# Performance work log

Measured on AMD Instinct MI355X. Metric: run time of the kernel, lower is better.

The kernel has to match this reference:

```python
import jax, jax.numpy as jnp
import numpy as np

B, H, A, T, C, MAXLEN = 128, 512, 128, 256, 256, 300
NEG_SLOPE = 0.01  # torch LeakyReLU default


def setup_inputs() -> dict:
    key = jax.random.key(0)
    ks = jax.random.split(key, 32)
    s = 0.02
    inp = {
        "key": jax.random.normal(ks[0], (B, A, T), jnp.float32),
        "value": jax.random.normal(ks[1], (B, T, A), jnp.float32),
        "Yinput": jax.random.randint(ks[2], (B, MAXLEN), 0, C),
        "frame_lens": jax.random.randint(ks[3], (B,), 1024, 2049),
        "max_len": MAXLEN,
        # parameters
        "emb": jax.random.normal(ks[4], (C, H), jnp.float32) * s,   # tied with projection
        "Wq": jax.random.normal(ks[5], (A, H), jnp.float32) * s,
        "bq": jnp.zeros((A,), jnp.float32),
        "Wih1": jax.random.normal(ks[6], (4 * H, H + A), jnp.float32) * s,
        "Whh1": jax.random.normal(ks[7], (4 * H, H), jnp.float32) * s,
        "bih1": jnp.zeros((4 * H,), jnp.float32),
        "bhh1": jnp.zeros((4 * H,), jnp.float32),
        "Wih2": jax.random.normal(ks[8], (4 * H, H), jnp.float32) * s,
        "Whh2": jax.random.normal(ks[9], (4 * H, H), jnp.float32) * s,
        "bih2": jnp.zeros((4 * H,), jnp.float32),
        "bhh2": jnp.zeros((4 * H,), jnp.float32),
        "Wih3": jax.random.normal(ks[10], (4 * H, H), jnp.float32) * s,
        "Whh3": jax.random.normal(ks[11], (4 * H, H), jnp.float32) * s,
        "bih3": jnp.zeros((4 * H,), jnp.float32),
        "bhh3": jnp.zeros((4 * H,), jnp.float32),
        "Wmlp": jax.random.normal(ks[12], (H, H + A), jnp.float32) * s,
        "bmlp": jnp.zeros((H,), jnp.float32),
        "bproj": jnp.zeros((C,), jnp.float32),
        "h00": jax.random.normal(ks[13], (1, H), jnp.float32) * s,
        "h01": jax.random.normal(ks[14], (1, H), jnp.float32) * s,
        "h02": jax.random.normal(ks[15], (1, H), jnp.float32) * s,
        "c00": jax.random.normal(ks[16], (1, H), jnp.float32) * s,
        "c01": jax.random.normal(ks[17], (1, H), jnp.float32) * s,
        "c02": jax.random.normal(ks[18], (1, H), jnp.float32) * s,
    }
    return inp


def _lstm_cell(x, h, c, Wih, Whh, bih, bhh):
    gates = x @ Wih.T + bih + h @ Whh.T + bhh  # [B,4H]
    i, f, g, o = jnp.split(gates, 4, axis=-1)
    i, f, o = jax.nn.sigmoid(i), jax.nn.sigmoid(f), jax.nn.sigmoid(o)
    g = jnp.tanh(g)
    c_new = f * c + i * g
    h_new = o * jnp.tanh(c_new)
    return h_new, c_new


def _attend(key, value, h, Wq, bq, mask):
    q = h @ Wq.T + bq                       # [B,A]
    energy = jnp.einsum('ba,bat->bt', q, key)  # [B,T]
    attn = jax.nn.softmax(energy, axis=-1)
    attn = attn * mask
    attn = attn / jnp.sum(attn, axis=-1, keepdims=True)
    ctx = jnp.einsum('bt,btv->bv', attn, value)  # [B,A]
    return ctx


def reference(key, value, Yinput, frame_lens, max_len,
              emb, Wq, bq,
              Wih1, Whh1, bih1, bhh1,
              Wih2, Whh2, bih2, bhh2,
              Wih3, Whh3, bih3, bhh3,
              Wmlp, bmlp, bproj,
              h00, h01, h02, c00, c01, c02):
    b, _, t = key.shape
    flens = frame_lens // 8
    mask = (jnp.arange(t)[None, :] < flens[:, None]).astype(key.dtype)  # [B,T]

    bc = lambda p: jnp.broadcast_to(p, (b, p.shape[-1]))
    h1, h2, h3 = bc(h00), bc(h01), bc(h02)
    c1, c2, c3 = bc(c00), bc(c01), bc(c02)
    ctx = _attend(key, value, h3, Wq, bq, mask)

    def step(carry, y_t):
        h1, h2, h3, c1, c2, c3, ctx = carry
        x = jnp.concatenate([emb[y_t], ctx], axis=-1)       # [B, H+A]
        h1, c1 = _lstm_cell(x, h1, c1, Wih1, Whh1, bih1, bhh1)
        h2, c2 = _lstm_cell(h1, h2, c2, Wih2, Whh2, bih2, bhh2)
        h3, c3 = _lstm_cell(h2, h3, c3, Wih3, Whh3, bih3, bhh3)
        ctx = _attend(key, value, h3, Wq, bq, mask)
        cat = jnp.concatenate([h3, ctx], axis=-1)           # [B, H+A]
        m = cat @ Wmlp.T + bmlp
        m = jnp.where(m >= 0, m, NEG_SLOPE * m)             # LeakyReLU
        logits = m @ emb.T + bproj                          # tied projection
        pred = jax.nn.log_softmax(logits, axis=-1)          # [B,C]
        return (h1, h2, h3, c1, c2, c3, ctx), pred

    ys = Yinput[:, :max_len].T                              # [max_len, B]
    _, preds = jax.lax.scan(step, (h1, h2, h3, c1, c2, c3, ctx), ys)
    return jnp.transpose(preds, (1, 0, 2))                  # [B, max_len, C]
```

## Files before the change

kernel.cpp:

```cpp
#include <hip/hip_runtime.h>

typedef unsigned short u16;
typedef unsigned int   u32;
typedef __bf16 bf16x8 __attribute__((ext_vector_type(8)));
typedef float  f32x4  __attribute__((ext_vector_type(4)));

#define NB 128
#define NH 512
#define NA 128
#define NT 256
#define NC 256
#define NL 300

static constexpr size_t OFF_BAR   = 0;
static constexpr size_t OFF_H1    = 4096;
static constexpr size_t OFF_H2    = OFF_H1   + 262144;
static constexpr size_t OFF_H3    = OFF_H2   + 262144;
static constexpr size_t OFF_C     = OFF_H3   + 262144;
static constexpr size_t OFF_CTX   = OFF_C    + 786432;
static constexpr size_t OFF_Q     = OFF_CTX  + 32768;
static constexpr size_t OFF_MP    = OFF_Q    + 65536;
static constexpr size_t OFF_M     = OFF_MP   + 262144;
static constexpr size_t OFF_LOG   = OFF_M    + 131072;
static constexpr size_t OFF_W1C   = OFF_LOG  + 131072;
static constexpr size_t OFF_WHH1  = OFF_W1C  + 524288;
static constexpr size_t OFF_WIH2  = OFF_WHH1 + 2097152;
static constexpr size_t OFF_WHH2  = OFF_WIH2 + 2097152;
static constexpr size_t OFF_WIH3  = OFF_WHH2 + 2097152;
static constexpr size_t OFF_WHH3  = OFF_WIH3 + 2097152;
static constexpr size_t OFF_WMH   = OFF_WHH3 + 2097152;
static constexpr size_t OFF_WMC   = OFF_WMH  + 524288;
static constexpr size_t OFF_WQ    = OFF_WMC  + 131072;
static constexpr size_t OFF_EMB   = OFF_WQ   + 131072;
static constexpr size_t OFF_PROJ1 = OFF_EMB  + 262144;
static constexpr size_t OFF_BS2   = OFF_PROJ1+ 1048576;
static constexpr size_t OFF_BS3   = OFF_BS2  + 8192;
static constexpr size_t OFF_KEY   = OFF_BS3  + 8192;
static constexpr size_t OFF_VAL   = OFF_KEY  + 8388608;
static constexpr size_t OFF_END   = OFF_VAL  + 8388608;

__device__ __forceinline__ u16 f2bf(float f) {
  u32 u = __builtin_bit_cast(u32, f);
  u32 r = (u + 0x7FFFu + ((u >> 16) & 1u)) >> 16;
  return (u16)r;
}
__device__ __forceinline__ float bf2f(u16 h) {
  return __builtin_bit_cast(float, ((u32)h) << 16);
}
__device__ __forceinline__ float sigm(float x) { return 1.f / (1.f + __expf(-x)); }
__device__ __forceinline__ float ftanh(float x) {
  x = fminf(fmaxf(x, -15.f), 15.f);
  float e = __expf(2.f * x);
  return (e - 1.f) / (e + 1.f);
}

__device__ __forceinline__ float ld_coh_f32(const float* p) {
  float v;
  asm volatile("global_load_dword %0, %1, off sc0 sc1\n\ts_waitcnt vmcnt(0)"
               : "=v"(v) : "v"(p) : "memory");
  return v;
}
__device__ __forceinline__ u32 ld_coh_u32(const u32* p) {
  u32 v;
  asm volatile("global_load_dword %0, %1, off sc0 sc1\n\ts_waitcnt vmcnt(0)"
               : "=v"(v) : "v"(p) : "memory");
  return v;
}
__device__ __forceinline__ f32x4 ld_coh16(const u16* p) {
  f32x4 v;
  asm volatile("global_load_dwordx4 %0, %1, off sc0 sc1\n\ts_waitcnt vmcnt(0)"
               : "=v"(v) : "v"(p) : "memory");
  return v;
}
__device__ __forceinline__ void ld_coh64(const u16* p, f32x4& a, f32x4& b, f32x4& c, f32x4& d) {
  asm volatile(
      "global_load_dwordx4 %0, %4, off sc0 sc1\n\t"
      "global_load_dwordx4 %1, %4, off offset:16 sc0 sc1\n\t"
      "global_load_dwordx4 %2, %4, off offset:32 sc0 sc1\n\t"
      "global_load_dwordx4 %3, %4, off offset:48 sc0 sc1\n\t"
      "s_waitcnt vmcnt(0)"
      : "=&v"(a), "=&v"(b), "=&v"(c), "=&v"(d)
      : "v"(p) : "memory");
}
__device__ __forceinline__ void st_coh_f32(float* p, float v) {
  asm volatile("global_store_dword %0, %1, off sc0 sc1" :: "v"(p), "v"(v) : "memory");
}
__device__ __forceinline__ void st_coh_bf16(u16* p, u16 v) {
  u32 vv = v;
  asm volatile("global_store_short %0, %1, off sc0 sc1" :: "v"(p), "v"(vv) : "memory");
}

__device__ __forceinline__ void gbar(char* ws, int xcd, u32& phase) {
  asm volatile("s_waitcnt vmcnt(0)" ::: "memory");
  __syncthreads();
  if (threadIdx.x == 0) {
    u32* cx = (u32*)(ws + OFF_BAR + 256 * (size_t)(1 + xcd));
    u32* cr = (u32*)(ws + OFF_BAR);
    ++phase;
    u32 prev = __hip_atomic_fetch_add(cx, 1u, __ATOMIC_RELAXED, __HIP_MEMORY_SCOPE_AGENT);
    if (prev == phase * 32u - 1u)
      __hip_atomic_fetch_add(cr, 1u, __ATOMIC_RELAXED, __HIP_MEMORY_SCOPE_AGENT);
    u32 tgt = phase * 8u;
    while (ld_coh_u32(cr) < tgt) __builtin_amdgcn_s_sleep(2);
  }
  __syncthreads();
}

__device__ __forceinline__ float wgmax(float v, float* s) {
#pragma unroll
  for (int o = 32; o; o >>= 1) v = fmaxf(v, __shfl_xor(v, o, 64));
  if ((threadIdx.x & 63) == 0) s[threadIdx.x >> 6] = v;
  __syncthreads();
  v = fmaxf(fmaxf(s[0], s[1]), fmaxf(s[2], s[3]));
  __syncthreads();
  return v;
}
__device__ __forceinline__ float wgsum(float v, float* s) {
#pragma unroll
  for (int o = 32; o; o >>= 1) v += __shfl_xor(v, o, 64);
  if ((threadIdx.x & 63) == 0) s[threadIdx.x >> 6] = v;
  __syncthreads();
  v = s[0] + s[1] + s[2] + s[3];
  __syncthreads();
  return v;
}

__device__ __forceinline__ void stage512(u16* sA, int lstride, int lcol0, const u16* src, int mt) {
  const int row = threadIdx.x >> 4;
  const int c4  = (threadIdx.x & 15) * 32;
  const u16* p = src + (((size_t)(mt * 16 + row)) << 9) + c4;
  f32x4 a, b, c, d;
  ld_coh64(p, a, b, c, d);
  f32x4* dst = (f32x4*)(sA + (size_t)row * lstride + lcol0 + c4);
  dst[0] = a; dst[1] = b; dst[2] = c; dst[3] = d;
}
__device__ __forceinline__ void stage128(u16* sA, int lstride, int lcol0, const u16* src, int mt) {
  const int row = threadIdx.x >> 4;
  const int c1  = (threadIdx.x & 15) * 8;
  const u16* p = src + (size_t)(mt * 16 + row) * 128 + c1;
  f32x4 a = ld_coh16(p);
  *(f32x4*)(sA + (size_t)row * lstride + lcol0 + c1) = a;
}

template <int NKS>
__device__ __forceinline__ f32x4 mm_part(f32x4 acc, const u16* sAp, int lstride, int lcol0,
                                         int ks0, const u16* W, int kw, int colbase, int lane) {
  const int ra = lane & 15, kg = lane >> 4;
  const u16* ap = sAp + (size_t)ra * lstride + lcol0 + kg * 8 + ks0 * 32;
  const u16* wp = W + (size_t)(colbase + ra) * kw + kg * 8 + (size_t)ks0 * 32;
#pragma unroll
  for (int k = 0; k < NKS; ++k) {
    bf16x8 av = *(const bf16x8*)(ap + k * 32);
    bf16x8 bv = *(const bf16x8*)(wp + k * 32);
    acc = __builtin_amdgcn_mfma_f32_16x16x32_bf16(av, bv, acc, 0, 0, 0);
  }
  return acc;
}
__device__ __forceinline__ void gx_write(float (*gx)[16][17], int wv, int lane, f32x4 acc) {
  const int col = lane & 15, r0 = (lane >> 4) * 4;
#pragma unroll
  for (int r = 0; r < 4; ++r) gx[wv][r0 + r][col] = acc[r];
}
__device__ __forceinline__ float gx_sum(float (*gx)[16][17], int bl, int jl) {
  return gx[0][bl][jl] + gx[1][bl][jl] + gx[2][bl][jl] + gx[3][bl][jl];
}

__device__ __forceinline__ void cell_update(int layer, int mt, int ut, int t,
                                            float (*gx)[16][17], const int* Yin,
                                            const u16* proj1, const float* bsum,
                                            float* CB, u16* hout) {
  const int bl = threadIdx.x >> 4, ul = threadIdx.x & 15;
  const int bg = mt * 16 + bl, ug = ut * 16 + ul;
  float iv = gx[0][bl][ul], fv = gx[1][bl][ul], gv = gx[2][bl][ul], ov = gx[3][bl][ul];
  if (proj1) {
    const int y = Yin[bg * NL + t];
    const u16* pr = proj1 + (size_t)y * 2048 + ug;
    iv += bf2f(pr[0]); fv += bf2f(pr[512]); gv += bf2f(pr[1024]); ov += bf2f(pr[1536]);
  } else {
    iv += bsum[ug]; fv += bsum[512 + ug]; gv += bsum[1024 + ug]; ov += bsum[1536 + ug];
  }
  float* cp = CB + ((size_t)layer * NB + bg) * NH + ug;
  const float c0 = *cp;
  const float ii = sigm(iv), ff = sigm(fv), gg = ftanh(gv), oo = sigm(ov);
  const float cn = ff * c0 + ii * gg;
  *cp = cn;
  st_coh_bf16(hout + (size_t)bg * NH + ug, f2bf(oo * ftanh(cn)));
}

__device__ __forceinline__ void mfin(int mt, int ut, const u16* sAc,
                                     const float* MP, const u16* WMC, u16* MB) {
  const int tid = threadIdx.x;
  const int jl = tid >> 4, bl = tid & 15;
  const int bg = mt * 16 + bl, j = ut * 16 + jl;
  float s = ld_coh_f32(MP + (size_t)bg * NH + j);
  const u16* wr = WMC + (size_t)j * NA;
  const u16* cr = sAc + (size_t)bl * 648;
#pragma unroll 8
  for (int k = 0; k < NA; ++k) s += bf2f(cr[k]) * bf2f(wr[k]);
  s = (s >= 0.f) ? s : 0.01f * s;
  st_coh_bf16(MB + (size_t)bg * NH + j, f2bf(s));
}

__device__ void attn_finish(int b, const float* QB, const int* flens,
                            const u16* KEY, const u16* VAL, u16* CTX, float* aux) {
  const int tid = threadIdx.x;
  if (tid < NA) aux[tid] = ld_coh_f32(QB + (size_t)b * NA + tid);
  __syncthreads();
  const int fl = flens[b] >> 3;
  float e = -3.0e38f;
  if (tid < fl) {
    e = 0.f;
    const u16* kp = KEY + (size_t)b * NA * NT + tid;
#pragma unroll 8
    for (int a = 0; a < NA; ++a) e += aux[a] * bf2f(kp[(size_t)a * NT]);
  }
  const float mx = wgmax(e, aux + 520);
  float ex = (tid < fl) ? __expf(e - mx) : 0.f;
  const float sm = wgsum(ex, aux + 520);
  aux[256 + tid] = ex / sm;
  __syncthreads();
  if (tid < NA) {
    float c = 0.f;
    const u16* vp = VAL + (size_t)b * NT * NA + tid;
#pragma unroll 8
    for (int t2 = 0; t2 < NT; ++t2) c += aux[256 + t2] * bf2f(vp[(size_t)t2 * NA]);
    st_coh_bf16(CTX + (size_t)b * NA + tid, f2bf(c));
  }
}

__device__ void lsm(int b, int tp, const float* LG, float* out, float* aux) {
  const int tid = threadIdx.x;
  const float l = ld_coh_f32(LG + (size_t)b * NC + tid);
  const float mx = wgmax(l, aux + 520);
  const float ex = __expf(l - mx);
  const float sm = wgsum(ex, aux + 520);
  out[((size_t)b * NL + tp) * NC + tid] = l - mx - __logf(sm);
}

__global__ void k_conv(const float* __restrict__ src, u16* __restrict__ dst,
                       int rows, int cols, int sstride, int soff) {
  const int n = rows * cols;
  for (int i = blockIdx.x * blockDim.x + threadIdx.x; i < n; i += gridDim.x * blockDim.x) {
    const int r = i / cols, c = i - r * cols;
    dst[i] = f2bf(src[(size_t)r * sstride + soff + c]);
  }
}

__global__ void k_proj1(const float* __restrict__ emb, const float* __restrict__ Wih1,
                        const float* __restrict__ bih1, const float* __restrict__ bhh1,
                        u16* __restrict__ proj) {
  __shared__ float se[8][512];
  const int c0 = (blockIdx.x >> 3) * 8;
  const int g = (blockIdx.x & 7) * 256 + threadIdx.x;
  for (int i = threadIdx.x; i < 4096; i += 256)
    se[i >> 9][i & 511] = emb[(size_t)(c0 + (i >> 9)) * NH + (i & 511)];
  __syncthreads();
  const float bb = bih1[g] + bhh1[g];
  const float* w = Wih1 + (size_t)g * 640;
  for (int cc = 0; cc < 8; ++cc) {
    float s = 0.f;
#pragma unroll 8
    for (int k = 0; k < 512; ++k) s += se[cc][k] * w[k];
    proj[(size_t)(c0 + cc) * 2048 + g] = f2bf(s + bb);
  }
}

__global__ void k_init(const float* h00, const float* h01, const float* h02,
                       const float* c00, const float* c01, const float* c02,
                       const float* bih2, const float* bhh2,
                       const float* bih3, const float* bhh3, char* ws) {
  const int i = blockIdx.x * 256 + threadIdx.x;
  u16* H1 = (u16*)(ws + OFF_H1);
  u16* H2 = (u16*)(ws + OFF_H2);
  u16* H3 = (u16*)(ws + OFF_H3);
  float* CB = (float*)(ws + OFF_C);
  const int k = i & 511;
  H1[i] = f2bf(h00[k]); H2[i] = f2bf(h01[k]); H3[i] = f2bf(h02[k]);
  CB[i] = c00[k]; CB[65536 + i] = c01[k]; CB[131072 + i] = c02[k];
  if (i < 2048) {
    ((float*)(ws + OFF_BS2))[i] = bih2[i] + bhh2[i];
    ((float*)(ws + OFF_BS3))[i] = bih3[i] + bhh3[i];
  }
  if (i < 1024) ((u32*)(ws + OFF_BAR))[i] = 0;
}

__global__ void __launch_bounds__(256, 1) k_dec(
    const int* __restrict__ Yin, const int* __restrict__ flens,
    const float* __restrict__ bq, const float* __restrict__ bmlp,
    const float* __restrict__ bproj, float* __restrict__ out, char* __restrict__ ws) {
  __shared__ __align__(16) u16 sA[16 * 1040];
  __shared__ float gx[4][16][17];
  __shared__ float aux[576];

  u16* H1 = (u16*)(ws + OFF_H1);
  u16* H2 = (u16*)(ws + OFF_H2);
  u16* H3 = (u16*)(ws + OFF_H3);
  float* CB = (float*)(ws + OFF_C);
  u16* CTX = (u16*)(ws + OFF_CTX);
  float* QB = (float*)(ws + OFF_Q);
  float* MP = (float*)(ws + OFF_MP);
  u16* MB = (u16*)(ws + OFF_M);
  float* LG = (float*)(ws + OFF_LOG);
  const u16* W1C  = (const u16*)(ws + OFF_W1C);
  const u16* WHH1 = (const u16*)(ws + OFF_WHH1);
  const u16* WIH2 = (const u16*)(ws + OFF_WIH2);
  const u16* WHH2 = (const u16*)(ws + OFF_WHH2);
  const u16* WIH3 = (const u16*)(ws + OFF_WIH3);
  const u16* WHH3 = (const u16*)(ws + OFF_WHH3);
  const u16* WMH  = (const u16*)(ws + OFF_WMH);
  const u16* WMC  = (const u16*)(ws + OFF_WMC);
  const u16* WQB  = (const u16*)(ws + OFF_WQ);
  const u16* EMBB = (const u16*)(ws + OFF_EMB);
  const u16* PJ1  = (const u16*)(ws + OFF_PROJ1);
  const float* BS2 = (const float*)(ws + OFF_BS2);
  const float* BS3 = (const float*)(ws + OFF_BS3);
  const u16* KEY = (const u16*)(ws + OFF_KEY);
  const u16* VAL = (const u16*)(ws + OFF_VAL);

  const int wg = blockIdx.x, tid = threadIdx.x;
  const int lane = tid & 63, wv = tid >> 6;
  const int xcd = wg & 7, slot = wg >> 3;
  const int ut = xcd * 4 + (slot >> 3);
  const int mt = slot & 7;
  u32 phase = 0;

  {
    stage512(sA, 520, 0, H3, mt);
    __syncthreads();
    if (ut < 8) {
      f32x4 acc = {0.f, 0.f, 0.f, 0.f};
      acc = mm_part<4>(acc, sA, 520, 0, wv * 4, WQB, 512, ut * 16, lane);
      gx_write(gx, wv, lane, acc);
    }
    __syncthreads();
    if (ut < 8) {
      const int bl = tid >> 4, jl = tid & 15;
      st_coh_f32(QB + (size_t)(mt * 16 + bl) * NA + ut * 16 + jl,
                 gx_sum(gx, bl, jl) + bq[ut * 16 + jl]);
    }
  }
  gbar(ws, xcd, phase);
  if (wg < NB) attn_finish(wg, QB, flens, KEY, VAL, CTX, aux);
  gbar(ws, xcd, phase);

  for (int t = 0; t < NL; ++t) {
    const int o = t & 1, n = o ^ 1;
    u16* h1o = H1 + o * 65536; u16* h1n = H1 + n * 65536;
    u16* h2o = H2 + o * 65536; u16* h2n = H2 + n * 65536;
    u16* h3o = H3 + o * 65536; u16* h3n = H3 + n * 65536;

    {
      stage128(sA, 648, 0, CTX, mt);
      stage512(sA, 648, 128, h1o, mt);
      __syncthreads();
      f32x4 acc = {0.f, 0.f, 0.f, 0.f};
      const int colbase = wv * 512 + ut * 16;
      acc = mm_part<4>(acc, sA, 648, 0, 0, W1C, 128, colbase, lane);
      acc = mm_part<16>(acc, sA, 648, 128, 0, WHH1, 512, colbase, lane);
      gx_write(gx, wv, lane, acc);
      __syncthreads();
      cell_update(0, mt, ut, t, gx, Yin, PJ1, nullptr, CB, h1n);
      if (t >= 1) mfin(mt, ut, sA, MP, WMC, MB);
    }
    gbar(ws, xcd, phase);

    {
      stage512(sA, 1032, 0, h1n, mt);
      stage512(sA, 1032, 512, h2o, mt);
      __syncthreads();
      f32x4 acc = {0.f, 0.f, 0.f, 0.f};
      const int colbase = wv * 512 + ut * 16;
      acc = mm_part<16>(acc, sA, 1032, 0, 0, WIH2, 512, colbase, lane);
      acc = mm_part<16>(acc, sA, 1032, 512, 0, WHH2, 512, colbase, lane);
      gx_write(gx, wv, lane, acc);
      __syncthreads();
      cell_update(1, mt, ut, t, gx, Yin, nullptr, BS2, CB, h2n);
    }
    gbar(ws, xcd, phase);

    {
      stage512(sA, 1032, 0, h2n, mt);
      stage512(sA, 1032, 512, h3o, mt);
      __syncthreads();
      f32x4 acc = {0.f, 0.f, 0.f, 0.f};
      const int colbase = wv * 512 + ut * 16;
      acc = mm_part<16>(acc, sA, 1032, 0, 0, WIH3, 512, colbase, lane);
      acc = mm_part<16>(acc, sA, 1032, 512, 0, WHH3, 512, colbase, lane);
      gx_write(gx, wv, lane, acc);
      __syncthreads();
      cell_update(2, mt, ut, t, gx, Yin, nullptr, BS3, CB, h3n);
    }
    gbar(ws, xcd, phase);

    {
      stage512(sA, 520, 0, h3n, mt);
      const bool dop = (ut >= 16) && (t >= 1);
      if (dop) stage512(sA + 16 * 520, 520, 0, MB, mt);
      __syncthreads();
      {
        f32x4 acc = {0.f, 0.f, 0.f, 0.f};
        acc = mm_part<4>(acc, sA, 520, 0, wv * 4, WMH, 512, ut * 16, lane);
        gx_write(gx, wv, lane, acc);
        __syncthreads();
        const int bl = tid >> 4, jl = tid & 15;
        st_coh_f32(MP + (size_t)(mt * 16 + bl) * NH + ut * 16 + jl,
                   gx_sum(gx, bl, jl) + bmlp[ut * 16 + jl]);
        __syncthreads();
      }
      if (ut < 8) {
        f32x4 acc = {0.f, 0.f, 0.f, 0.f};
        acc = mm_part<4>(acc, sA, 520, 0, wv * 4, WQB, 512, ut * 16, lane);
        gx_write(gx, wv, lane, acc);
        __syncthreads();
        const int bl = tid >> 4, jl = tid & 15;
        st_coh_f32(QB + (size_t)(mt * 16 + bl) * NA + ut * 16 + jl,
                   gx_sum(gx, bl, jl) + bq[ut * 16 + jl]);
      }
      if (dop) {
        f32x4 acc = {0.f, 0.f, 0.f, 0.f};
        acc = mm_part<4>(acc, sA + 16 * 520, 520, 0, wv * 4, EMBB, 512, (ut - 16) * 16, lane);
        gx_write(gx, wv, lane, acc);
        __syncthreads();
        const int bl = tid >> 4, jl = tid & 15;
        st_coh_f32(LG + (size_t)(mt * 16 + bl) * NC + (ut - 16) * 16 + jl,
                   gx_sum(gx, bl, jl) + bproj[(ut - 16) * 16 + jl]);
      }
    }
    gbar(ws, xcd, phase);

    if (wg < NB)          attn_finish(wg, QB, flens, KEY, VAL, CTX, aux);
    else if (t >= 1)      lsm(wg - NB, t - 1, LG, out, aux);
    gbar(ws, xcd, phase);
  }

  {
    stage128(sA, 648, 0, CTX, mt);
    __syncthreads();
    mfin(mt, ut, sA, MP, WMC, MB);
  }
  gbar(ws, xcd, phase);
  {
    if (ut >= 16) stage512(sA, 520, 0, MB, mt);
    __syncthreads();
    if (ut >= 16) {
      f32x4 acc = {0.f, 0.f, 0.f, 0.f};
      acc = mm_part<4>(acc, sA, 520, 0, wv * 4, EMBB, 512, (ut - 16) * 16, lane);
      gx_write(gx, wv, lane, acc);
      __syncthreads();
      const int bl = tid >> 4, jl = tid & 15;
      st_coh_f32(LG + (size_t)(mt * 16 + bl) * NC + (ut - 16) * 16 + jl,
                 gx_sum(gx, bl, jl) + bproj[(ut - 16) * 16 + jl]);
    }
  }
  gbar(ws, xcd, phase);
  if (wg >= NB) lsm(wg - NB, NL - 1, LG, out, aux);
}

extern "C" void kernel_launch(void* const* d_in, const int* in_sizes, int n_in,
                              void* d_out, int out_size, void* d_ws, size_t ws_size,
                              hipStream_t stream) {
  (void)in_sizes; (void)n_in; (void)out_size;
  if (ws_size < OFF_END) return;

  const float* key   = (const float*)d_in[0];
  const float* value = (const float*)d_in[1];
  const int*   Yin   = (const int*)d_in[2];
  const int*   flens = (const int*)d_in[3];
  const float* emb   = (const float*)d_in[5];
  const float* Wq    = (const float*)d_in[6];
  const float* bq    = (const float*)d_in[7];
  const float* Wih1  = (const float*)d_in[8];
  const float* Whh1  = (const float*)d_in[9];
  const float* bih1  = (const float*)d_in[10];
  const float* bhh1  = (const float*)d_in[11];
  const float* Wih2  = (const float*)d_in[12];
  const float* Whh2  = (const float*)d_in[13];
  const float* bih2  = (const float*)d_in[14];
  const float* bhh2  = (const float*)d_in[15];
  const float* Wih3  = (const float*)d_in[16];
  const float* Whh3  = (const float*)d_in[17];
  const float* bih3  = (const float*)d_in[18];
  const float* bhh3  = (const float*)d_in[19];
  const float* Wmlp  = (const float*)d_in[20];
  const float* bmlp  = (const float*)d_in[21];
  const float* bproj = (const float*)d_in[22];
  const float* h00   = (const float*)d_in[23];
  const float* h01   = (const float*)d_in[24];
  const float* h02   = (const float*)d_in[25];
  const float* c00   = (const float*)d_in[26];
  const float* c01   = (const float*)d_in[27];
  const float* c02   = (const float*)d_in[28];
  float* out = (float*)d_out;
  char* ws = (char*)d_ws;

  dim3 cb(256);
#define CONV(src, off, r, c, ss, so) \
  k_conv<<<512, cb, 0, stream>>>(src, (u16*)(ws + off), r, c, ss, so)
  CONV(Whh1,  OFF_WHH1, 2048, 512, 512, 0);
  CONV(Wih1,  OFF_W1C,  2048, 128, 640, 512);
  CONV(Wih2,  OFF_WIH2, 2048, 512, 512, 0);
  CONV(Whh2,  OFF_WHH2, 2048, 512, 512, 0);
  CONV(Wih3,  OFF_WIH3, 2048, 512, 512, 0);
  CONV(Whh3,  OFF_WHH3, 2048, 512, 512, 0);
  CONV(Wmlp,  OFF_WMH,  512, 512, 640, 0);
  CONV(Wmlp,  OFF_WMC,  512, 128, 640, 512);
  CONV(Wq,    OFF_WQ,   128, 512, 512, 0);
  CONV(emb,   OFF_EMB,  256, 512, 512, 0);
  CONV(key,   OFF_KEY,  16384, 256, 256, 0);
  CONV(value, OFF_VAL,  32768, 128, 128, 0);
#undef CONV
  k_proj1<<<256, cb, 0, stream>>>(emb, Wih1, bih1, bhh1, (u16*)(ws + OFF_PROJ1));
  k_init<<<256, cb, 0, stream>>>(h00, h01, h02, c00, c01, c02,
                                 bih2, bhh2, bih3, bhh3, ws);
  k_dec<<<256, cb, 0, stream>>>(Yin, flens, bq, bmlp, bproj, out, ws);
}
```

Measured before the change: 16.96 ms.

## Localize grid barriers per batch tile and fuse attention into decoder phases

Reassigns work groups so each batch tile of 16 rows is owned by 32 consecutive groups, letting the grid barrier become a per-tile counter rather than a two-level global barrier. Attention (query projection, scores, context) now runs per batch row inside the fourth phase, using key and value transposed up front so reads are contiguous. The MLP-context part and the logits projection are folded into earlier phases, and log-softmax runs in the layer-3 phase, which removes one barrier per timestep. Staging loads are issued together before a single wait so their latencies overlap. The cost is heavier per-group attention work, a busy-spin barrier without sleep, and a larger shared-memory footprint.

```diff
diff --git a/kernel.cpp b/kernel.cpp
--- a/kernel.cpp
+++ b/kernel.cpp
@@ -11,6 +11,7 @@
 #define NT 256
 #define NC 256
 #define NL 300
+#define SA 1544
 
 static constexpr size_t OFF_BAR   = 0;
 static constexpr size_t OFF_H1    = 4096;
@@ -72,15 +73,23 @@
                : "=v"(v) : "v"(p) : "memory");
   return v;
 }
-__device__ __forceinline__ void ld_coh64(const u16* p, f32x4& a, f32x4& b, f32x4& c, f32x4& d) {
+__device__ __forceinline__ void ld4_issue(const u16* p, f32x4& a, f32x4& b, f32x4& c, f32x4& d) {
   asm volatile(
       "global_load_dwordx4 %0, %4, off sc0 sc1\n\t"
       "global_load_dwordx4 %1, %4, off offset:16 sc0 sc1\n\t"
       "global_load_dwordx4 %2, %4, off offset:32 sc0 sc1\n\t"
-      "global_load_dwordx4 %3, %4, off offset:48 sc0 sc1\n\t"
-      "s_waitcnt vmcnt(0)"
+      "global_load_dwordx4 %3, %4, off offset:48 sc0 sc1"
       : "=&v"(a), "=&v"(b), "=&v"(c), "=&v"(d)
       : "v"(p) : "memory");
+}
+__device__ __forceinline__ void ld1_issue(const u16* p, f32x4& a) {
+  asm volatile("global_load_dwordx4 %0, %1, off sc0 sc1" : "=&v"(a) : "v"(p) : "memory");
+}
+__device__ __forceinline__ void ldf_issue(const float* p, float& v) {
+  asm volatile("global_load_dword %0, %1, off sc0 sc1" : "=&v"(v) : "v"(p) : "memory");
+}
+__device__ __forceinline__ void vm_wait() {
+  asm volatile("s_waitcnt vmcnt(0)" ::: "memory");
 }
 __device__ __forceinline__ void st_coh_f32(float* p, float v) {
   asm volatile("global_store_dword %0, %1, off sc0 sc1" :: "v"(p), "v"(v) : "memory");
@@ -90,18 +99,15 @@
   asm volatile("global_store_short %0, %1, off sc0 sc1" :: "v"(p), "v"(vv) : "memory");
 }
 
-__device__ __forceinline__ void gbar(char* ws, int xcd, u32& phase) {
+__device__ __forceinline__ void gbar(char* ws, int grp, u32& phase) {
   asm volatile("s_waitcnt vmcnt(0)" ::: "memory");
   __syncthreads();
   if (threadIdx.x == 0) {
-    u32* cx = (u32*)(ws + OFF_BAR + 256 * (size_t)(1 + xcd));
-    u32* cr = (u32*)(ws + OFF_BAR);
+    u32* c = (u32*)(ws + OFF_BAR + 256 * (size_t)grp);
     ++phase;
-    u32 prev = __hip_atomic_fetch_add(cx, 1u, __ATOMIC_RELAXED, __HIP_MEMORY_SCOPE_AGENT);
-    if (prev == phase * 32u - 1u)
-      __hip_atomic_fetch_add(cr, 1u, __ATOMIC_RELAXED, __HIP_MEMORY_SCOPE_AGENT);
-    u32 tgt = phase * 8u;
-    while (ld_coh_u32(cr) < tgt) __builtin_amdgcn_s_sleep(2);
+    __hip_atomic_fetch_add(c, 1u, __ATOMIC_RELAXED, __HIP_MEMORY_SCOPE_AGENT);
+    const u32 tgt = phase * 32u;
+    while (ld_coh_u32(c) < tgt) { }
   }
   __syncthreads();
 }
@@ -125,28 +131,22 @@
   return v;
 }
 
-__device__ __forceinline__ void stage512(u16* sA, int lstride, int lcol0, const u16* src, int mt) {
-  const int row = threadIdx.x >> 4;
-  const int c4  = (threadIdx.x & 15) * 32;
+__device__ __forceinline__ void stage512_issue(const u16* src, int mt, f32x4* r) {
+  const int row = threadIdx.x >> 4, c4 = (threadIdx.x & 15) * 32;
   const u16* p = src + (((size_t)(mt * 16 + row)) << 9) + c4;
-  f32x4 a, b, c, d;
-  ld_coh64(p, a, b, c, d);
-  f32x4* dst = (f32x4*)(sA + (size_t)row * lstride + lcol0 + c4);
-  dst[0] = a; dst[1] = b; dst[2] = c; dst[3] = d;
-}
-__device__ __forceinline__ void stage128(u16* sA, int lstride, int lcol0, const u16* src, int mt) {
-  const int row = threadIdx.x >> 4;
-  const int c1  = (threadIdx.x & 15) * 8;
-  const u16* p = src + (size_t)(mt * 16 + row) * 128 + c1;
-  f32x4 a = ld_coh16(p);
-  *(f32x4*)(sA + (size_t)row * lstride + lcol0 + c1) = a;
+  ld4_issue(p, r[0], r[1], r[2], r[3]);
+}
+__device__ __forceinline__ void stage512_write(u16* sA, int lcol0, f32x4* r) {
+  const int row = threadIdx.x >> 4, c4 = (threadIdx.x & 15) * 32;
+  f32x4* dst = (f32x4*)(sA + (size_t)row * SA + lcol0 + c4);
+  dst[0] = r[0]; dst[1] = r[1]; dst[2] = r[2]; dst[3] = r[3];
 }
 
 template <int NKS>
-__device__ __forceinline__ f32x4 mm_part(f32x4 acc, const u16* sAp, int lstride, int lcol0,
+__device__ __forceinline__ f32x4 mm_part(f32x4 acc, const u16* sAp, int lcol0,
                                          int ks0, const u16* W, int kw, int colbase, int lane) {
   const int ra = lane & 15, kg = lane >> 4;
-  const u16* ap = sAp + (size_t)ra * lstride + lcol0 + kg * 8 + ks0 * 32;
+  const u16* ap = sAp + (size_t)ra * SA + lcol0 + kg * 8 + ks0 * 32;
   const u16* wp = W + (size_t)(colbase + ra) * kw + kg * 8 + (size_t)ks0 * 32;
 #pragma unroll
   for (int k = 0; k < NKS; ++k) {
@@ -187,43 +187,54 @@
   st_coh_bf16(hout + (size_t)bg * NH + ug, f2bf(oo * ftanh(cn)));
 }
 
-__device__ __forceinline__ void mfin(int mt, int ut, const u16* sAc,
-                                     const float* MP, const u16* WMC, u16* MB) {
+__device__ void attn2(int b, const u16* h3row, const int* flens, const u16* WQ,
+                      const u16* KT, const u16* VT, u16* CTX, const float* bq,
+                      u16* hq, float* aux) {
   const int tid = threadIdx.x;
-  const int jl = tid >> 4, bl = tid & 15;
-  const int bg = mt * 16 + bl, j = ut * 16 + jl;
-  float s = ld_coh_f32(MP + (size_t)bg * NH + j);
-  const u16* wr = WMC + (size_t)j * NA;
-  const u16* cr = sAc + (size_t)bl * 648;
+  if (tid < 64) {
+    f32x4 v = ld_coh16(h3row + tid * 8);
+    *(f32x4*)(hq + tid * 8) = v;
+  }
+  __syncthreads();
+  if (tid < NA) {
+    const bf16x8* wr = (const bf16x8*)(WQ + (size_t)tid * NH);
+    float qv = bq[tid];
 #pragma unroll 8
-  for (int k = 0; k < NA; ++k) s += bf2f(cr[k]) * bf2f(wr[k]);
-  s = (s >= 0.f) ? s : 0.01f * s;
-  st_coh_bf16(MB + (size_t)bg * NH + j, f2bf(s));
-}
-
-__device__ void attn_finish(int b, const float* QB, const int* flens,
-                            const u16* KEY, const u16* VAL, u16* CTX, float* aux) {
-  const int tid = threadIdx.x;
-  if (tid < NA) aux[tid] = ld_coh_f32(QB + (size_t)b * NA + tid);
+    for (int k8 = 0; k8 < 64; ++k8) {
+      bf16x8 w8 = wr[k8];
+#pragma unroll
+      for (int kk = 0; kk < 8; ++kk) qv += bf2f(hq[k8 * 8 + kk]) * (float)w8[kk];
+    }
+    aux[tid] = qv;
+  }
   __syncthreads();
   const int fl = flens[b] >> 3;
   float e = -3.0e38f;
-  if (tid < fl) {
-    e = 0.f;
-    const u16* kp = KEY + (size_t)b * NA * NT + tid;
-#pragma unroll 8
-    for (int a = 0; a < NA; ++a) e += aux[a] * bf2f(kp[(size_t)a * NT]);
-  }
-  const float mx = wgmax(e, aux + 520);
+  {
+    const bf16x8* kr = (const bf16x8*)(KT + ((size_t)b * NT + tid) * NA);
+    float s = 0.f;
+#pragma unroll
+    for (int k8 = 0; k8 < 16; ++k8) {
+      bf16x8 kv = __builtin_nontemporal_load(kr + k8);
+#pragma unroll
+      for (int kk = 0; kk < 8; ++kk) s += aux[k8 * 8 + kk] * (float)kv[kk];
+    }
+    if (tid < fl) e = s;
+  }
+  const float mx = wgmax(e, aux + 400);
   float ex = (tid < fl) ? __expf(e - mx) : 0.f;
-  const float sm = wgsum(ex, aux + 520);
-  aux[256 + tid] = ex / sm;
+  const float sm = wgsum(ex, aux + 400);
+  aux[128 + tid] = ex / sm;
   __syncthreads();
   if (tid < NA) {
+    const bf16x8* vr = (const bf16x8*)(VT + ((size_t)b * NA + tid) * NT);
     float c = 0.f;
-    const u16* vp = VAL + (size_t)b * NT * NA + tid;
-#pragma unroll 8
-    for (int t2 = 0; t2 < NT; ++t2) c += aux[256 + t2] * bf2f(vp[(size_t)t2 * NA]);
+#pragma unroll
+    for (int k8 = 0; k8 < 32; ++k8) {
+      bf16x8 vv = __builtin_nontemporal_load(vr + k8);
+#pragma unroll
+      for (int kk = 0; kk < 8; ++kk) c += aux[128 + k8 * 8 + kk] * (float)vv[kk];
+    }
     st_coh_bf16(CTX + (size_t)b * NA + tid, f2bf(c));
   }
 }
@@ -231,9 +242,9 @@
 __device__ void lsm(int b, int tp, const float* LG, float* out, float* aux) {
   const int tid = threadIdx.x;
   const float l = ld_coh_f32(LG + (size_t)b * NC + tid);
-  const float mx = wgmax(l, aux + 520);
+  const float mx = wgmax(l, aux + 400);
   const float ex = __expf(l - mx);
-  const float sm = wgsum(ex, aux + 520);
+  const float sm = wgsum(ex, aux + 400);
   out[((size_t)b * NL + tp) * NC + tid] = l - mx - __logf(sm);
 }
 
@@ -244,6 +255,22 @@
     const int r = i / cols, c = i - r * cols;
     dst[i] = f2bf(src[(size_t)r * sstride + soff + c]);
   }
+}
+
+__global__ void k_trans(const float* __restrict__ src, u16* __restrict__ dst, int R, int C) {
+  __shared__ float tile[32][33];
+  const int rt = R >> 5, ct = C >> 5;
+  const int bid = blockIdx.x;
+  const int b = bid / (rt * ct), rem = bid % (rt * ct);
+  const int r0 = (rem / ct) * 32, c0 = (rem % ct) * 32;
+  const int tr = threadIdx.x >> 5, tc = threadIdx.x & 31;
+  const float* s = src + ((size_t)b * R + r0) * C + c0;
+#pragma unroll
+  for (int i = 0; i < 4; ++i) tile[tr + i * 8][tc] = s[(size_t)(tr + i * 8) * C + tc];
+  __syncthreads();
+  u16* d = dst + ((size_t)b * C + c0) * R + r0;
+#pragma unroll
+  for (int i = 0; i < 4; ++i) d[(size_t)(tr + i * 8) * R + tc] = f2bf(tile[tc][tr + i * 8]);
 }
 
 __global__ void k_proj1(const float* __restrict__ emb, const float* __restrict__ Wih1,
@@ -288,16 +315,16 @@
     const int* __restrict__ Yin, const int* __restrict__ flens,
     const float* __restrict__ bq, const float* __restrict__ bmlp,
     const float* __restrict__ bproj, float* __restrict__ out, char* __restrict__ ws) {
-  __shared__ __align__(16) u16 sA[16 * 1040];
+  __shared__ __align__(16) u16 sA[16 * SA];
   __shared__ float gx[4][16][17];
-  __shared__ float aux[576];
+  __shared__ float aux[416];
+  __shared__ __align__(16) u16 hq[512];
 
   u16* H1 = (u16*)(ws + OFF_H1);
   u16* H2 = (u16*)(ws + OFF_H2);
   u16* H3 = (u16*)(ws + OFF_H3);
   float* CB = (float*)(ws + OFF_C);
   u16* CTX = (u16*)(ws + OFF_CTX);
-  float* QB = (float*)(ws + OFF_Q);
   float* MP = (float*)(ws + OFF_MP);
   u16* MB = (u16*)(ws + OFF_M);
   float* LG = (float*)(ws + OFF_LOG);
@@ -314,34 +341,20 @@
   const u16* PJ1  = (const u16*)(ws + OFF_PROJ1);
   const float* BS2 = (const float*)(ws + OFF_BS2);
   const float* BS3 = (const float*)(ws + OFF_BS3);
-  const u16* KEY = (const u16*)(ws + OFF_KEY);
-  const u16* VAL = (const u16*)(ws + OFF_VAL);
+  const u16* KT = (const u16*)(ws + OFF_KEY);
+  const u16* VT = (const u16*)(ws + OFF_VAL);
 
   const int wg = blockIdx.x, tid = threadIdx.x;
   const int lane = tid & 63, wv = tid >> 6;
-  const int xcd = wg & 7, slot = wg >> 3;
-  const int ut = xcd * 4 + (slot >> 3);
-  const int mt = slot & 7;
+  const int mt = wg >> 5;
+  const int ut = wg & 31;
+  const int bl = tid >> 4, jl = tid & 15;
   u32 phase = 0;
 
-  {
-    stage512(sA, 520, 0, H3, mt);
-    __syncthreads();
-    if (ut < 8) {
-      f32x4 acc = {0.f, 0.f, 0.f, 0.f};
-      acc = mm_part<4>(acc, sA, 520, 0, wv * 4, WQB, 512, ut * 16, lane);
-      gx_write(gx, wv, lane, acc);
-    }
-    __syncthreads();
-    if (ut < 8) {
-      const int bl = tid >> 4, jl = tid & 15;
-      st_coh_f32(QB + (size_t)(mt * 16 + bl) * NA + ut * 16 + jl,
-                 gx_sum(gx, bl, jl) + bq[ut * 16 + jl]);
-    }
-  }
-  gbar(ws, xcd, phase);
-  if (wg < NB) attn_finish(wg, QB, flens, KEY, VAL, CTX, aux);
-  gbar(ws, xcd, phase);
+  if (ut >= 16)
+    attn2(mt * 16 + (ut - 16), H3 + (size_t)(mt * 16 + (ut - 16)) * NH,
+          flens, WQB, KT, VT, CTX, bq, hq, aux);
+  gbar(ws, mt, phase);
 
   for (int t = 0; t < NL; ++t) {
     const int o = t & 1, n = o ^ 1;
@@ -350,110 +363,149 @@
     u16* h3o = H3 + o * 65536; u16* h3n = H3 + n * 65536;
 
     {
-      stage128(sA, 648, 0, CTX, mt);
-      stage512(sA, 648, 128, h1o, mt);
+      f32x4 rc, rh[4]; float mpv = 0.f;
+      { const int row = tid >> 4, c1 = (tid & 15) * 8;
+        ld1_issue(CTX + (size_t)(mt * 16 + row) * NA + c1, rc); }
+      stage512_issue(h1o, mt, rh);
+      if (t >= 1) ldf_issue(MP + (size_t)(mt * 16 + bl) * NH + ut * 16 + jl, mpv);
+      vm_wait();
+      { const int row = tid >> 4, c1 = (tid & 15) * 8;
+        *(f32x4*)(sA + (size_t)row * SA + c1) = rc; }
+      stage512_write(sA, 128, rh);
       __syncthreads();
       f32x4 acc = {0.f, 0.f, 0.f, 0.f};
       const int colbase = wv * 512 + ut * 16;
-      acc = mm_part<4>(acc, sA, 648, 0, 0, W1C, 128, colbase, lane);
-      acc = mm_part<16>(acc, sA, 648, 128, 0, WHH1, 512, colbase, lane);
+      acc = mm_part<4>(acc, sA, 0, 0, W1C, 128, colbase, lane);
+      acc = mm_part<16>(acc, sA, 128, 0, WHH1, 512, colbase, lane);
       gx_write(gx, wv, lane, acc);
       __syncthreads();
       cell_update(0, mt, ut, t, gx, Yin, PJ1, nullptr, CB, h1n);
-      if (t >= 1) mfin(mt, ut, sA, MP, WMC, MB);
-    }
-    gbar(ws, xcd, phase);
+      __syncthreads();
+      if (t >= 1) {
+        f32x4 a2 = {0.f, 0.f, 0.f, 0.f};
+        a2 = mm_part<1>(a2, sA, 0, wv, WMC, 128, ut * 16, lane);
+        gx_write(gx, wv, lane, a2);
+      }
+      __syncthreads();
+      if (t >= 1) {
+        float s = gx_sum(gx, bl, jl) + mpv;
+        s = (s >= 0.f) ? s : 0.01f * s;
+        st_coh_bf16(MB + (size_t)(mt * 16 + bl) * NH + ut * 16 + jl, f2bf(s));
+      }
+    }
+    gbar(ws, mt, phase);
 
     {
-      stage512(sA, 1032, 0, h1n, mt);
-      stage512(sA, 1032, 512, h2o, mt);
+      f32x4 r1[4], r2[4], r3[4];
+      stage512_issue(h1n, mt, r1);
+      stage512_issue(h2o, mt, r2);
+      const bool dop = (ut >= 16) && (t >= 1);
+      if (dop) stage512_issue(MB, mt, r3);
+      vm_wait();
+      stage512_write(sA, 0, r1);
+      stage512_write(sA, 512, r2);
+      if (dop) stage512_write(sA, 1024, r3);
       __syncthreads();
       f32x4 acc = {0.f, 0.f, 0.f, 0.f};
       const int colbase = wv * 512 + ut * 16;
-      acc = mm_part<16>(acc, sA, 1032, 0, 0, WIH2, 512, colbase, lane);
-      acc = mm_part<16>(acc, sA, 1032, 512, 0, WHH2, 512, colbase, lane);
+      acc = mm_part<16>(acc, sA, 0, 0, WIH2, 512, colbase, lane);
+      acc = mm_part<16>(acc, sA, 512, 0, WHH2, 512, colbase, lane);
       gx_write(gx, wv, lane, acc);
       __syncthreads();
       cell_update(1, mt, ut, t, gx, Yin, nullptr, BS2, CB, h2n);
-    }
-    gbar(ws, xcd, phase);
+      __syncthreads();
+      if (dop) {
+        f32x4 a2 = {0.f, 0.f, 0.f, 0.f};
+        a2 = mm_part<4>(a2, sA, 1024, wv * 4, EMBB, 512, (ut - 16) * 16, lane);
+        gx_write(gx, wv, lane, a2);
+      }
+      __syncthreads();
+      if (dop)
+        st_coh_f32(LG + (size_t)(mt * 16 + bl) * NC + (ut - 16) * 16 + jl,
+                   gx_sum(gx, bl, jl) + bproj[(ut - 16) * 16 + jl]);
+    }
+    gbar(ws, mt, phase);
 
     {
-      stage512(sA, 1032, 0, h2n, mt);
-      stage512(sA, 1032, 512, h3o, mt);
+      f32x4 r1[4], r2[4];
+      stage512_issue(h2n, mt, r1);
+      stage512_issue(h3o, mt, r2);
+      vm_wait();
+      stage512_write(sA, 0, r1);
+      stage512_write(sA, 512, r2);
       __syncthreads();
       f32x4 acc = {0.f, 0.f, 0.f, 0.f};
       const int colbase = wv * 512 + ut * 16;
-      acc = mm_part<16>(acc, sA, 1032, 0, 0, WIH3, 512, colbase, lane);
-      acc = mm_part<16>(acc, sA, 1032, 512, 0, WHH3, 512, colbase, lane);
+      acc = mm_part<16>(acc, sA, 0, 0, WIH3, 512, colbase, lane);
+      acc = mm_part<16>(acc, sA, 512, 0, WHH3, 512, colbase, lane);
       gx_write(gx, wv, lane, acc);
       __syncthreads();
       cell_update(2, mt, ut, t, gx, Yin, nullptr, BS3, CB, h3n);
-    }
-    gbar(ws, xcd, phase);
+      if (ut < 16 && t >= 1) lsm(mt * 16 + ut, t - 1, LG, out, aux);
+    }
+    gbar(ws, mt, phase);
 
     {
-      stage512(sA, 520, 0, h3n, mt);
-      const bool dop = (ut >= 16) && (t >= 1);
-      if (dop) stage512(sA + 16 * 520, 520, 0, MB, mt);
-      __syncthreads();
-      {
-        f32x4 acc = {0.f, 0.f, 0.f, 0.f};
-        acc = mm_part<4>(acc, sA, 520, 0, wv * 4, WMH, 512, ut * 16, lane);
-        gx_write(gx, wv, lane, acc);
+      if (ut < 16) {
+        f32x4 rh[4];
+        stage512_issue(h3n, mt, rh);
+        vm_wait();
+        stage512_write(sA, 0, rh);
         __syncthreads();
-        const int bl = tid >> 4, jl = tid & 15;
-        st_coh_f32(MP + (size_t)(mt * 16 + bl) * NH + ut * 16 + jl,
-                   gx_sum(gx, bl, jl) + bmlp[ut * 16 + jl]);
-        __syncthreads();
+#pragma unroll
+        for (int half = 0; half < 2; ++half) {
+          const int cb = ut * 32 + half * 16;
+          f32x4 acc = {0.f, 0.f, 0.f, 0.f};
+          acc = mm_part<4>(acc, sA, 0, wv * 4, WMH, 512, cb, lane);
+          gx_write(gx, wv, lane, acc);
+          __syncthreads();
+          st_coh_f32(MP + (size_t)(mt * 16 + bl) * NH + cb + jl,
+                     gx_sum(gx, bl, jl) + bmlp[cb + jl]);
+          __syncthreads();
+        }
+      } else {
+        const int b = mt * 16 + (ut - 16);
+        attn2(b, h3n + (size_t)b * NH, flens, WQB, KT, VT, CTX, bq, hq, aux);
       }
-      if (ut < 8) {
-        f32x4 acc = {0.f, 0.f, 0.f, 0.f};
-        acc = mm_part<4>(acc, sA, 520, 0, wv * 4, WQB, 512, ut * 16, lane);
-        gx_write(gx, wv, lane, acc);
-        __syncthreads();
-        const int bl = tid >> 4, jl = tid & 15;
-        st_coh_f32(QB + (size_t)(mt * 16 + bl) * NA + ut * 16 + jl,
-                   gx_sum(gx, bl, jl) + bq[ut * 16 + jl]);
-      }
-      if (dop) {
-        f32x4 acc = {0.f, 0.f, 0.f, 0.f};
-        acc = mm_part<4>(acc, sA + 16 * 520, 520, 0, wv * 4, EMBB, 512, (ut - 16) * 16, lane);
-        gx_write(gx, wv, lane, acc);
-        __syncthreads();
-        const int bl = tid >> 4, jl = tid & 15;
-        st_coh_f32(LG + (size_t)(mt * 16 + bl) * NC + (ut - 16) * 16 + jl,
-                   gx_sum(gx, bl, jl) + bproj[(ut - 16) * 16 + jl]);
-      }
-    }
-    gbar(ws, xcd, phase);
-
-    if (wg < NB)          attn_finish(wg, QB, flens, KEY, VAL, CTX, aux);
-    else if (t >= 1)      lsm(wg - NB, t - 1, LG, out, aux);
-    gbar(ws, xcd, phase);
+    }
+    gbar(ws, mt, phase);
   }
 
   {
-    stage128(sA, 648, 0, CTX, mt);
+    f32x4 rc; float mpv = 0.f;
+    { const int row = tid >> 4, c1 = (tid & 15) * 8;
+      ld1_issue(CTX + (size_t)(mt * 16 + row) * NA + c1, rc); }
+    ldf_issue(MP + (size_t)(mt * 16 + bl) * NH + ut * 16 + jl, mpv);
+    vm_wait();
+    { const int row = tid >> 4, c1 = (tid & 15) * 8;
+      *(f32x4*)(sA + (size_t)row * SA + c1) = rc; }
     __syncthreads();
-    mfin(mt, ut, sA, MP, WMC, MB);
-  }
-  gbar(ws, xcd, phase);
+    f32x4 a2 = {0.f, 0.f, 0.f, 0.f};
+    a2 = mm_part<1>(a2, sA, 0, wv, WMC, 128, ut * 16, lane);
+    gx_write(gx, wv, lane, a2);
+    __syncthreads();
+    float s = gx_sum(gx, bl, jl) + mpv;
+    s = (s >= 0.f) ? s : 0.01f * s;
+    st_coh_bf16(MB + (size_t)(mt * 16 + bl) * NH + ut * 16 + jl, f2bf(s));
+  }
+  gbar(ws, mt, phase);
   {
-    if (ut >= 16) stage512(sA, 520, 0, MB, mt);
-    __syncthreads();
     if (ut >= 16) {
-      f32x4 acc = {0.f, 0.f, 0.f, 0.f};
-      acc = mm_part<4>(acc, sA, 520, 0, wv * 4, EMBB, 512, (ut - 16) * 16, lane);
-      gx_write(gx, wv, lane, acc);
-      __syncthreads();
-      const int bl = tid >> 4, jl = tid & 15;
+      f32x4 r3[4];
+      stage512_issue(MB, mt, r3);
+      vm_wait();
+      stage512_write(sA, 0, r3);
+      __syncthreads();
+      f32x4 a2 = {0.f, 0.f, 0.f, 0.f};
+      a2 = mm_part<4>(a2, sA, 0, wv * 4, EMBB, 512, (ut - 16) * 16, lane);
+      gx_write(gx, wv, lane, a2);
+      __syncthreads();
       st_coh_f32(LG + (size_t)(mt * 16 + bl) * NC + (ut - 16) * 16 + jl,
                  gx_sum(gx, bl, jl) + bproj[(ut - 16) * 16 + jl]);
     }
   }
-  gbar(ws, xcd, phase);
-  if (wg >= NB) lsm(wg - NB, NL - 1, LG, out, aux);
+  gbar(ws, mt, phase);
+  if (ut < 16) lsm(mt * 16 + ut, NL - 1, LG, out, aux);
 }
 
 extern "C" void kernel_launch(void* const* d_in, const int* in_sizes, int n_in,
@@ -506,9 +558,9 @@
   CONV(Wmlp,  OFF_WMC,  512, 128, 640, 512);
   CONV(Wq,    OFF_WQ,   128, 512, 512, 0);
   CONV(emb,   OFF_EMB,  256, 512, 512, 0);
-  CONV(key,   OFF_KEY,  16384, 256, 256, 0);
-  CONV(value, OFF_VAL,  32768, 128, 128, 0);
 #undef CONV
+  k_trans<<<4096, cb, 0, stream>>>(key,   (u16*)(ws + OFF_KEY), 128, 256);
+  k_trans<<<4096, cb, 0, stream>>>(value, (u16*)(ws + OFF_VAL), 256, 128);
   k_proj1<<<256, cb, 0, stream>>>(emb, Wih1, bih1, bhh1, (u16*)(ws + OFF_PROJ1));
   k_init<<<256, cb, 0, stream>>>(h00, h01, h02, c00, c01, c02,
                                  bih2, bhh2, bih3, bhh3, ws);
```

After: 16.83 ms. No clear change (-0.8%).
